# Optimization experiments

Hardware: AMD Instinct MI355X
Metric: run time of the kernel (lower is better)

The kernel has to match this reference:

```python
import jax, jax.numpy as jnp
import numpy as np

DIM = 192
HEADS = 8
EPS = 1e-12  # torch F.normalize eps


def setup_inputs() -> dict:
    key = jax.random.key(0)
    k1, k2, k3, k4 = jax.random.split(key, 4)
    b, c, h, w = 2, DIM, 256, 256
    x = jax.random.normal(k1, (b, c, h, w), dtype=jnp.float32)
    # 1x1 conv weights stored as (out, in)
    qkv_w = jax.random.normal(k2, (3 * c, c), dtype=jnp.float32) * (1.0 / np.sqrt(c))
    # depthwise 3x3, groups = 3c -> OIHW with I=1
    dw_w = jax.random.normal(k3, (3 * c, 1, 3, 3), dtype=jnp.float32) * (1.0 / 3.0)
    proj_w = jax.random.normal(k4, (c, c), dtype=jnp.float32) * (1.0 / np.sqrt(c))
    temperature = jnp.ones((HEADS, 1, 1), dtype=jnp.float32)
    return {"x": x, "qkv_w": qkv_w, "dw_w": dw_w, "proj_w": proj_w,
            "temperature": temperature}


def _l2norm(t):
    n = jnp.sqrt(jnp.sum(t * t, axis=-1, keepdims=True))
    return t / jnp.maximum(n, EPS)


def reference(x, qkv_w, dw_w, proj_w, temperature):
    b, c, h, w = x.shape
    # 1x1 conv (pointwise) -> depthwise 3x3 conv
    qkv = jnp.einsum('oc,bchw->bohw', qkv_w, x)  # (b, 3c, h, w)
    qkv = jax.lax.conv_general_dilated(
        qkv, dw_w, window_strides=(1, 1), padding='SAME',
        feature_group_count=3 * c,
        dimension_numbers=('NCHW', 'OIHW', 'NCHW'))
    q, k, v = jnp.split(qkv, 3, axis=1)
    # faithful reshape: full C channels per head, spatial dim split by heads
    q = q.reshape(b, HEADS, c, -1)
    k = k.reshape(b, HEADS, c, -1)
    v = v.reshape(b, HEADS, c, -1)
    q = _l2norm(q)
    k = _l2norm(k)
    attn = jnp.einsum('bhcn,bhdn->bhcd', q, k) * temperature  # (b,H,c,c)
    attn = jax.nn.softmax(attn, axis=-1)
    out = jnp.einsum('bhcd,bhdn->bhcn', attn, v)
    out = out.reshape(b, c, h, w)
    out = jnp.einsum('oc,bchw->bohw', proj_w, out)
    return out
```

## Files before the change

kernel.cpp:

```cpp
#include <hip/hip_runtime.h>
#include <math.h>

typedef unsigned short u16;
typedef unsigned int   u32;
typedef short bf16x8 __attribute__((ext_vector_type(8)));
typedef float f32x4  __attribute__((ext_vector_type(4)));

#define MFMA16(a,b,c) __builtin_amdgcn_mfma_f32_16x16x32_bf16((a),(b),(c),0,0,0)

__device__ __forceinline__ float bf2f(u16 h){ u32 u=((u32)h)<<16; return __uint_as_float(u); }
__device__ __forceinline__ u16 f2bf(float f){ u32 u=__float_as_uint(f); return (u16)((u+0x7fffu+((u>>16)&1u))>>16); }

__device__ __forceinline__ void gl2lds(const u16* g, u16* l){
  __builtin_amdgcn_global_load_lds((const __attribute__((address_space(1))) u32*)g,
                                   (__attribute__((address_space(3))) u32*)l, 16, 0, 0);
}
__device__ __forceinline__ void stc(u16* p, float v){ *p = f2bf(v); }
__device__ __forceinline__ void stc(float* p, float v){ *p = v; }
__device__ __forceinline__ void ld4(const float* p, float* v){ float4 x=*(const float4*)p; v[0]=x.x;v[1]=x.y;v[2]=x.z;v[3]=x.w; }
__device__ __forceinline__ void ld4(const u16* p, float* v){ ushort4 x=*(const ushort4*)p; v[0]=bf2f(x.x);v[1]=bf2f(x.y);v[2]=bf2f(x.z);v[3]=bf2f(x.w); }

__device__ __forceinline__ int xcd_remap(){
  int gx = gridDim.x, gy = gridDim.y;
  int lin = blockIdx.x + gx*(blockIdx.y + gy*blockIdx.z);
  int nwg = gx*gy*gridDim.z;
  if (nwg & 7) return lin;
  int q = nwg >> 3;
  return (lin & 7)*q + (lin >> 3);
}

__global__ void prep_kernel(const float* __restrict__ qkv_w, const float* __restrict__ proj_w,
                            u16* __restrict__ wq, u16* __restrict__ wp, float* __restrict__ norms){
  int i = blockIdx.x*256 + threadIdx.x;
  if (i < 110592) wq[i] = f2bf(qkv_w[i]);
  else if (i < 147456) wp[i-110592] = f2bf(proj_w[i-110592]);
  else if (i < 156672) norms[i-147456] = 0.f;
}

template<typename TIN>
__global__ __launch_bounds__(256) void transpose_kernel(
    const TIN* __restrict__ in, u16* __restrict__ out,
    long in_hi, long in_lo, long out_slab, int in_pitch)
{
  __shared__ float tile[64][65];
  const int t = threadIdx.x;
  const int z = blockIdx.z;
  const TIN* ip = in + (long)(z>>3)*in_hi + (long)(z&7)*in_lo;
  u16* op = out + (long)z*out_slab;
  const int s0 = blockIdx.x*64, c0 = blockIdx.y*64;
  const int rl = t>>4, cc = (t&15)*4;
#pragma unroll
  for (int rr=0; rr<4; rr++){
    int row = rr*16 + rl;
    float v[4];
    ld4(ip + (long)(c0+row)*in_pitch + s0 + cc, v);
    tile[row][cc+0]=v[0]; tile[row][cc+1]=v[1]; tile[row][cc+2]=v[2]; tile[row][cc+3]=v[3];
  }
  __syncthreads();
#pragma unroll
  for (int wr=0; wr<4; wr++){
    int sl = wr*16 + rl;
    ushort4 s;
    s.x = f2bf(tile[cc+0][sl]); s.y = f2bf(tile[cc+1][sl]);
    s.z = f2bf(tile[cc+2][sl]); s.w = f2bf(tile[cc+3][sl]);
    *(ushort4*)(op + (long)(s0+sl)*192 + c0 + cc) = s;
  }
}

template<typename TC>
__global__ __launch_bounds__(256) void gemm_nt_kernel(
    const u16* __restrict__ A, const u16* __restrict__ B, TC* __restrict__ C,
    int M, long sB, long sC)
{
  __shared__ __align__(16) u16 As[128*32];
  __shared__ __align__(16) u16 Bs[128*32];
  const int t = threadIdx.x, w = t>>6, l = t&63;
  const int wrk = xcd_remap();
  const int mt = wrk % gridDim.x;
  const int rest = wrk / gridDim.x;
  const int nt = rest % gridDim.y, bz = rest / gridDim.y;
  const int m0 = mt*128, n0 = nt*128;
  const u16* Bb = B + (long)bz*sB + (long)n0*192;
  const int rq = t>>2, qq = (t&3)*8;
  int ar0 = m0 + rq;      if (ar0 >= M) ar0 = M-1;
  int ar1 = m0 + 64 + rq; if (ar1 >= M) ar1 = M-1;
  f32x4 acc[4][4];
#pragma unroll
  for (int i=0;i<4;i++)
#pragma unroll
    for (int j=0;j<4;j++) acc[i][j] = f32x4{0.f,0.f,0.f,0.f};

  for (int k0=0; k0<192; k0+=32){
    __syncthreads();
    gl2lds(A + (long)ar0*192 + k0 + qq, As + t*8);
    gl2lds(A + (long)ar1*192 + k0 + qq, As + (256+t)*8);
    gl2lds(Bb + (long)rq*192 + k0 + qq, Bs + t*8);
    gl2lds(Bb + (long)(64+rq)*192 + k0 + qq, Bs + (256+t)*8);
    __syncthreads();
    const u16* ap = As + ((w>>1)*64 + (l&15))*32 + (l>>4)*8;
    const u16* bp = Bs + ((w&1)*64 + (l&15))*32 + (l>>4)*8;
    bf16x8 a[4], b[4];
#pragma unroll
    for (int i=0;i<4;i++){ a[i] = *(const bf16x8*)(ap + i*512); b[i] = *(const bf16x8*)(bp + i*512); }
#pragma unroll
    for (int i=0;i<4;i++)
#pragma unroll
      for (int j=0;j<4;j++) acc[i][j] = MFMA16(a[i], b[j], acc[i][j]);
  }
  const int mw = m0 + (w>>1)*64, nw = n0 + (w&1)*64;
  TC* Cb = C + (long)bz*sC;
#pragma unroll
  for (int i=0;i<4;i++){
#pragma unroll
    for (int r=0;r<4;r++){
      int row = mw + i*16 + (l>>4)*4 + r;
      if (row < M){
        TC* cp = Cb + (long)row*65536 + nw + (l&15);
#pragma unroll
        for (int j=0;j<4;j++) stc(cp + j*16, acc[i][j][r]);
      }
    }
  }
}

__global__ __launch_bounds__(256) void dwconv_kernel(
    const u16* __restrict__ in, const float* __restrict__ w9s,
    u16* __restrict__ out, float* __restrict__ norms)
{
  const int bo = blockIdx.x >> 2;
  const int rg = blockIdx.x & 3;
  const int o  = bo % 576;
  const int t = threadIdx.x, wv = t>>6, l = t&63;
  const u16* ip = in + (long)bo*65536L + l*4;
  u16* op = out + (long)bo*65536L + l*4;
  float w[9];
#pragma unroll
  for (int i=0;i<9;i++) w[i] = w9s[o*9+i];
  const int r0 = rg*64 + wv*16;
  float ap0=0.f,ap1=0.f,ap2=0.f,ap3=0.f;
  float ac0=0.f,ac1=0.f,ac2=0.f,ac3=0.f;
  float an0,an1,an2,an3;
  float ss = 0.f;
#pragma unroll
  for (int it=0; it<18; ++it){
    const int g = r0 - 1 + it;
    float v0,v1,v2,v3;
    if (g>=0 && g<256){
      ushort4 u = *(const ushort4*)(ip + g*256);
      v0=bf2f(u.x); v1=bf2f(u.y); v2=bf2f(u.z); v3=bf2f(u.w);
    } else { v0=0.f; v1=0.f; v2=0.f; v3=0.f; }
    float sl = __shfl(v3, (l+63)&63);
    float sr = __shfl(v0, (l+1)&63);
    const float lf  = (l==0)  ? 0.f : sl;
    const float rgt = (l==63) ? 0.f : sr;
    ap0 = fmaf(w[6],lf, fmaf(w[7],v0, fmaf(w[8],v1, ap0)));
    ap1 = fmaf(w[6],v0, fmaf(w[7],v1, fmaf(w[8],v2, ap1)));
    ap2 = fmaf(w[6],v1, fmaf(w[7],v2, fmaf(w[8],v3, ap2)));
    ap3 = fmaf(w[6],v2, fmaf(w[7],v3, fmaf(w[8],rgt, ap3)));
    if (it >= 2){
      ushort4 s;
      s.x = f2bf(ap0); s.y = f2bf(ap1); s.z = f2bf(ap2); s.w = f2bf(ap3);
      *(ushort4*)(op + (g-1)*256) = s;
      ss = fmaf(ap0,ap0, fmaf(ap1,ap1, fmaf(ap2,ap2, fmaf(ap3,ap3, ss))));
    }
    ac0 = fmaf(w[3],lf, fmaf(w[4],v0, fmaf(w[5],v1, ac0)));
    ac1 = fmaf(w[3],v0, fmaf(w[4],v1, fmaf(w[5],v2, ac1)));
    ac2 = fmaf(w[3],v1, fmaf(w[4],v2, fmaf(w[5],v3, ac2)));
    ac3 = fmaf(w[3],v2, fmaf(w[4],v3, fmaf(w[5],rgt, ac3)));
    an0 = fmaf(w[0],lf, fmaf(w[1],v0, w[2]*v1));
    an1 = fmaf(w[0],v0, fmaf(w[1],v1, w[2]*v2));
    an2 = fmaf(w[0],v1, fmaf(w[1],v2, w[2]*v3));
    an3 = fmaf(w[0],v2, fmaf(w[1],v3, w[2]*rgt));
    ap0=ac0; ap1=ac1; ap2=ac2; ap3=ac3;
    ac0=an0; ac1=an1; ac2=an2; ac3=an3;
  }
#pragma unroll
  for (int off=32; off>=1; off>>=1) ss += __shfl_xor(ss, off);
  if (o < 384 && l == 0){
    atomicAdd(&norms[bo*8 + (r0>>5)], ss);
  }
}

__global__ __launch_bounds__(256) void gemm_qk_kernel(
    const u16* __restrict__ conv, float* __restrict__ part)
{
  __shared__ __align__(16) u16 As[64*64];
  __shared__ __align__(16) u16 Bs[64*64];
  const int t = threadIdx.x, w = t>>6, l = t&63;
  const int wrk = xcd_remap();
  const int mt = wrk % 3;
  const int rest = wrk / 3;
  const int nt = rest % 3, z = rest / 3;
  const int bh = z>>3, sl = z&7;
  const int b = bh>>3, h = bh&7;
  const u16* Q  = conv + (long)b*37748736L + (long)h*1572864L;
  const u16* Kp = Q + 12582912L;
  const int m0 = mt*64, n0 = nt*64;
  const int rq = t>>3, qq = (t&7)*8;
  const long qo0 = (long)(m0+rq)*8192 + qq;
  const long qo1 = (long)(m0+32+rq)*8192 + qq;
  const long ko0 = (long)(n0+rq)*8192 + qq;
  const long ko1 = (long)(n0+32+rq)*8192 + qq;
  f32x4 acc[2][2];
#pragma unroll
  for (int i=0;i<2;i++)
#pragma unroll
    for (int j=0;j<2;j++) acc[i][j] = f32x4{0.f,0.f,0.f,0.f};
  const int kbeg = sl*1024;
  for (int k0=kbeg; k0<kbeg+1024; k0+=64){
    __syncthreads();
    gl2lds(Q  + qo0 + k0, As + t*8);
    gl2lds(Q  + qo1 + k0, As + (256+t)*8);
    gl2lds(Kp + ko0 + k0, Bs + t*8);
    gl2lds(Kp + ko1 + k0, Bs + (256+t)*8);
    __syncthreads();
    const u16* ap = As + ((w>>1)*32 + (l&15))*64 + (l>>4)*8;
    const u16* bp = Bs + ((w&1)*32 + (l&15))*64 + (l>>4)*8;
#pragma unroll
    for (int ks=0; ks<2; ks++){
      bf16x8 a0 = *(const bf16x8*)(ap + ks*32);
      bf16x8 a1 = *(const bf16x8*)(ap + 1024 + ks*32);
      bf16x8 b0 = *(const bf16x8*)(bp + ks*32);
      bf16x8 b1 = *(const bf16x8*)(bp + 1024 + ks*32);
      acc[0][0]=MFMA16(a0,b0,acc[0][0]); acc[0][1]=MFMA16(a0,b1,acc[0][1]);
      acc[1][0]=MFMA16(a1,b0,acc[1][0]); acc[1][1]=MFMA16(a1,b1,acc[1][1]);
    }
  }
  float* P = part + (long)z*36864L;
  const int mw = m0 + (w>>1)*32, nw = n0 + (w&1)*32;
#pragma unroll
  for (int i=0;i<2;i++)
#pragma unroll
    for (int j=0;j<2;j++)
#pragma unroll
      for (int r=0;r<4;r++)
        P[(long)(mw + i*16 + (l>>4)*4 + r)*192 + nw + j*16 + (l&15)] = acc[i][j][r];
}

__global__ __launch_bounds__(256) void softmax_kernel(
    const float* __restrict__ part, const float* __restrict__ temp,
    const float* __restrict__ norms, u16* __restrict__ attn)
{
  const int t = threadIdx.x, wv = t>>6, l = t&63;
  const int rg = blockIdx.x*4 + wv;
  const int bh = rg/192, r = rg - bh*192;
  const int b = bh>>3, h = bh&7;
  const float tp = temp[h];
  const float sq = norms[(b*576 + 24*h + (r>>3))*8 + (r&7)];
  const float invq = 1.f/fmaxf(sqrtf(sq), 1e-12f);
  const float* P = part + (long)bh*8L*36864L + (long)r*192;
  float lv[3];
#pragma unroll
  for (int j=0;j<3;j++){
    int col = l + j*64;
    float s = 0.f;
#pragma unroll
    for (int ks=0; ks<8; ks++) s += P[(long)ks*36864L + col];
    float sk = norms[(b*576 + 192 + 24*h + (col>>3))*8 + (col&7)];
    float invk = 1.f/fmaxf(sqrtf(sk), 1e-12f);
    lv[j] = s*invq*invk*tp;
  }
  float mx = fmaxf(lv[0], fmaxf(lv[1], lv[2]));
#pragma unroll
  for (int o=32;o>=1;o>>=1) mx = fmaxf(mx, __shfl_xor(mx, o));
  float e[3], sum = 0.f;
#pragma unroll
  for (int j=0;j<3;j++){ e[j] = expf(lv[j]-mx); sum += e[j]; }
#pragma unroll
  for (int o=32;o>=1;o>>=1) sum += __shfl_xor(sum, o);
  const float inv = 1.f/sum;
  u16* ap = attn + (long)bh*36864L + (long)r*192;
#pragma unroll
  for (int j=0;j<3;j++) ap[l + j*64] = f2bf(e[j]*inv);
}

__global__ __launch_bounds__(256) void gemm_av_kernel(
    const u16* __restrict__ VT, const u16* __restrict__ attn, u16* __restrict__ out_sc)
{
  __shared__ __align__(16) char smem[69632];
  u16* As = (u16*)smem;
  u16* Bs = (u16*)(smem + 8192);
  const int t = threadIdx.x, w = t>>6, l = t&63;
  const int wrk = xcd_remap();
  const int mt = wrk % 64;
  const int rest = wrk / 64;
  const int nt = rest % 2, bh = rest / 2;
  const int b = bh>>3, h = bh&7;
  const u16* Av = VT + (long)bh*1572864L;
  const u16* Bt = attn + (long)bh*36864L;
  const int m0 = mt*128, n0 = nt*128;
  const int rq = t>>2, qq = (t&3)*8;
  int br0 = n0 + rq;      if (br0 > 191) br0 = 191;
  int br1 = n0 + 64 + rq; if (br1 > 191) br1 = 191;
  f32x4 acc[4][4];
#pragma unroll
  for (int i=0;i<4;i++)
#pragma unroll
    for (int j=0;j<4;j++) acc[i][j] = f32x4{0.f,0.f,0.f,0.f};
  for (int k0=0; k0<192; k0+=32){
    __syncthreads();
    gl2lds(Av + (long)(m0+rq)*192 + k0 + qq, As + t*8);
    gl2lds(Av + (long)(m0+64+rq)*192 + k0 + qq, As + (256+t)*8);
    gl2lds(Bt + (long)br0*192 + k0 + qq, Bs + t*8);
    gl2lds(Bt + (long)br1*192 + k0 + qq, Bs + (256+t)*8);
    __syncthreads();
    const u16* ap = As + ((w>>1)*64 + (l&15))*32 + (l>>4)*8;
    const u16* bp = Bs + ((w&1)*64 + (l&15))*32 + (l>>4)*8;
    bf16x8 a[4], bb[4];
#pragma unroll
    for (int i=0;i<4;i++){ a[i] = *(const bf16x8*)(ap + i*512); bb[i] = *(const bf16x8*)(bp + i*512); }
#pragma unroll
    for (int i=0;i<4;i++)
#pragma unroll
      for (int j=0;j<4;j++) acc[i][j] = MFMA16(a[i], bb[j], acc[i][j]);
  }
  __syncthreads();
  float* wb = (float*)smem + w*4352;
#pragma unroll
  for (int i=0;i<4;i++)
#pragma unroll
    for (int j=0;j<4;j++)
#pragma unroll
      for (int r=0;r<4;r++)
        wb[(i*16 + (l>>4)*4 + r)*68 + j*16 + (l&15)] = acc[i][j][r];
  __syncthreads();
  const int c0w = nt*128 + (w&1)*64;
  if (c0w < 192){
    const int cb = 24*h + (c0w>>3);
    const int mw = m0 + (w>>1)*64;
    u16* ob = out_sc + (long)b*12582912L + cb;
    const int nl0 = l>>3, sb = l&7;
#pragma unroll
    for (int ri=0; ri<8; ri++){
      int nl = ri*8 + nl0;
      const float* src = wb + nl*68 + sb;
      u32 d0 = (u32)f2bf(src[0])  | ((u32)f2bf(src[8])  << 16);
      u32 d1 = (u32)f2bf(src[16]) | ((u32)f2bf(src[24]) << 16);
      u32 d2 = (u32)f2bf(src[32]) | ((u32)f2bf(src[40]) << 16);
      u32 d3 = (u32)f2bf(src[48]) | ((u32)f2bf(src[56]) << 16);
      *(uint4*)(ob + ((long)sb*8192 + mw + nl)*192) = make_uint4(d0,d1,d2,d3);
    }
  }
}

extern "C" void kernel_launch(void* const* d_in, const int* in_sizes, int n_in,
                              void* d_out, int out_size, void* d_ws, size_t ws_size,
                              hipStream_t stream)
{
  const float* x      = (const float*)d_in[0];
  const float* qkv_w  = (const float*)d_in[1];
  const float* dw_w   = (const float*)d_in[2];
  const float* proj_w = (const float*)d_in[3];
  const float* temp   = (const float*)d_in[4];
  float* out = (float*)d_out;

  char* ws = (char*)d_ws;
  u16*   xT      = (u16*)(ws + 0);
  u16*   conv    = (u16*)(ws + 0);
  u16*   qkv_raw = (u16*)(ws + 150994944);
  u16*   VT      = (u16*)(ws + 150994944);
  u16*   out_sc  = (u16*)(ws + 201326592);
  float* part    = (float*)(ws + 251658240);
  u16*   attn    = (u16*)(ws + 270532608);
  u16*   wq_bf   = (u16*)(ws + 301989888);
  u16*   wp_bf   = (u16*)(ws + 302211072);
  float* norms   = (float*)(ws + 302284800);

  prep_kernel<<<dim3(612), 256, 0, stream>>>(qkv_w, proj_w, wq_bf, wp_bf, norms);

  transpose_kernel<float><<<dim3(1024, 3, 2), 256, 0, stream>>>(
      x, xT, 0L, 12582912L, 12582912L, 65536);

  gemm_nt_kernel<u16><<<dim3(5, 512, 2), 256, 0, stream>>>(
      wq_bf, xT, qkv_raw, 576, 12582912L, 37748736L);

  dwconv_kernel<<<dim3(1152*4), 256, 0, stream>>>(qkv_raw, dw_w, conv, norms);

  transpose_kernel<u16><<<dim3(128, 3, 16), 256, 0, stream>>>(
      conv + 25165824L, VT, 37748736L, 1572864L, 1572864L, 8192);

  gemm_qk_kernel<<<dim3(3, 3, 128), 256, 0, stream>>>(conv, part);

  softmax_kernel<<<dim3(768), 256, 0, stream>>>(part, temp, norms, attn);

  gemm_av_kernel<<<dim3(64, 2, 16), 256, 0, stream>>>(VT, attn, out_sc);

  gemm_nt_kernel<float><<<dim3(2, 512, 2), 256, 0, stream>>>(
      wp_bf, out_sc, out, 192, 12582912L, 12582912L);
}
```

Baseline: 464.0 us.

## Fuse input transpose into QKV GEMM and widen depthwise conv per-thread work

Removes the separate fp32-to-bf16 transpose of x by having the QKV GEMM load fp32 x tiles directly into swizzled LDS and convert them to bf16 when building B fragments. This drops a full write and read of the transposed input. The depthwise conv now processes 8 columns per thread over 16 rows with half the blocks, and writes the norm partials directly instead of using atomics. The trade-off is twice the LDS traffic for the fp32 B tile plus per-element conversion inside the GEMM inner loop.

```diff
diff --git a/kernel.cpp b/kernel.cpp
--- a/kernel.cpp
+++ b/kernel.cpp
@@ -5,6 +5,7 @@
 typedef unsigned int   u32;
 typedef short bf16x8 __attribute__((ext_vector_type(8)));
 typedef float f32x4  __attribute__((ext_vector_type(4)));
+typedef u16 u16x8 __attribute__((ext_vector_type(8)));
 
 #define MFMA16(a,b,c) __builtin_amdgcn_mfma_f32_16x16x32_bf16((a),(b),(c),0,0,0)
 
@@ -37,15 +38,14 @@
   else if (i < 156672) norms[i-147456] = 0.f;
 }
 
-template<typename TIN>
 __global__ __launch_bounds__(256) void transpose_kernel(
-    const TIN* __restrict__ in, u16* __restrict__ out,
+    const u16* __restrict__ in, u16* __restrict__ out,
     long in_hi, long in_lo, long out_slab, int in_pitch)
 {
   __shared__ float tile[64][65];
   const int t = threadIdx.x;
   const int z = blockIdx.z;
-  const TIN* ip = in + (long)(z>>3)*in_hi + (long)(z&7)*in_lo;
+  const u16* ip = in + (long)(z>>3)*in_hi + (long)(z&7)*in_lo;
   u16* op = out + (long)z*out_slab;
   const int s0 = blockIdx.x*64, c0 = blockIdx.y*64;
   const int rl = t>>4, cc = (t&15)*4;
@@ -64,6 +64,77 @@
     s.x = f2bf(tile[cc+0][sl]); s.y = f2bf(tile[cc+1][sl]);
     s.z = f2bf(tile[cc+2][sl]); s.w = f2bf(tile[cc+3][sl]);
     *(ushort4*)(op + (long)(s0+sl)*192 + c0 + cc) = s;
+  }
+}
+
+__global__ __launch_bounds__(256) void gemm_qkv_kernel(
+    const u16* __restrict__ A, const float* __restrict__ X, u16* __restrict__ C)
+{
+  __shared__ __align__(16) u16 As[128*32];
+  __shared__ __align__(16) float Bs[32*128];
+  const int t = threadIdx.x, w = t>>6, l = t&63;
+  const int wrk = xcd_remap();
+  const int mt = wrk % 5;
+  const int rest = wrk / 5;
+  const int nt = rest % 512, bz = rest / 512;
+  const int m0 = mt*128, n0 = nt*128;
+  const float* Xb = X + (long)bz*12582912L + n0;
+  const int rq = t>>2, qq = (t&3)*8;
+  int ar0 = m0 + rq;      if (ar0 >= 576) ar0 = 575;
+  int ar1 = m0 + 64 + rq; if (ar1 >= 576) ar1 = 575;
+  const int brow = t>>5;
+  const int bcs0 = t&31;
+  f32x4 acc[4][4];
+#pragma unroll
+  for (int i=0;i<4;i++)
+#pragma unroll
+    for (int j=0;j<4;j++) acc[i][j] = f32x4{0.f,0.f,0.f,0.f};
+
+  for (int k0=0; k0<192; k0+=32){
+    __syncthreads();
+    gl2lds(A + (long)ar0*192 + k0 + qq, As + t*8);
+    gl2lds(A + (long)ar1*192 + k0 + qq, As + (256+t)*8);
+#pragma unroll
+    for (int i=0;i<4;i++){
+      const int r  = i*8 + brow;
+      const int cs = bcs0 ^ (i<<2);
+      gl2lds((const u16*)(Xb + (long)(k0+r)*65536 + cs*4),
+             (u16*)Bs + (i*256+t)*8);
+    }
+    __syncthreads();
+    const u16* ap = As + ((w>>1)*64 + (l&15))*32 + (l>>4)*8;
+    const int kg = l>>4;
+    const int colb = (w&1)*64 + (l&15);
+    bf16x8 a[4], b[4];
+#pragma unroll
+    for (int i=0;i<4;i++) a[i] = *(const bf16x8*)(ap + i*512);
+#pragma unroll
+    for (int j=0;j<4;j++){
+      const int col = colb + j*16;
+      const float* bp = Bs + kg*1024 + ((((col>>2) ^ (kg<<2))<<2) + (col&3));
+      bf16x8 bv;
+#pragma unroll
+      for (int jj=0;jj<8;jj++) bv[jj] = (short)f2bf(bp[jj*128]);
+      b[j] = bv;
+    }
+#pragma unroll
+    for (int i=0;i<4;i++)
+#pragma unroll
+      for (int j=0;j<4;j++) acc[i][j] = MFMA16(a[i], b[j], acc[i][j]);
+  }
+  const int mw = m0 + (w>>1)*64, nw = n0 + (w&1)*64;
+  u16* Cb = C + (long)bz*37748736L;
+#pragma unroll
+  for (int i=0;i<4;i++){
+#pragma unroll
+    for (int r=0;r<4;r++){
+      int row = mw + i*16 + (l>>4)*4 + r;
+      if (row < 576){
+        u16* cp = Cb + (long)row*65536 + nw + (l&15);
+#pragma unroll
+        for (int j=0;j<4;j++) stc(cp + j*16, acc[i][j][r]);
+      }
+    }
   }
 }
 
@@ -127,58 +198,59 @@
     const u16* __restrict__ in, const float* __restrict__ w9s,
     u16* __restrict__ out, float* __restrict__ norms)
 {
-  const int bo = blockIdx.x >> 2;
-  const int rg = blockIdx.x & 3;
+  const int bo = blockIdx.x >> 1;
+  const int half = blockIdx.x & 1;
   const int o  = bo % 576;
   const int t = threadIdx.x, wv = t>>6, l = t&63;
-  const u16* ip = in + (long)bo*65536L + l*4;
-  u16* op = out + (long)bo*65536L + l*4;
+  const int q = l&31;
+  const int r0 = half*128 + wv*32 + (l>>5)*16;
+  const u16* ip = in + (long)bo*65536L + q*8;
+  u16* op = out + (long)bo*65536L + q*8;
   float w[9];
 #pragma unroll
   for (int i=0;i<9;i++) w[i] = w9s[o*9+i];
-  const int r0 = rg*64 + wv*16;
-  float ap0=0.f,ap1=0.f,ap2=0.f,ap3=0.f;
-  float ac0=0.f,ac1=0.f,ac2=0.f,ac3=0.f;
-  float an0,an1,an2,an3;
+  float ap[8], ac[8], an[8];
+#pragma unroll
+  for (int c=0;c<8;c++){ ap[c]=0.f; ac[c]=0.f; }
   float ss = 0.f;
 #pragma unroll
   for (int it=0; it<18; ++it){
     const int g = r0 - 1 + it;
-    float v0,v1,v2,v3;
+    float v[8];
     if (g>=0 && g<256){
-      ushort4 u = *(const ushort4*)(ip + g*256);
-      v0=bf2f(u.x); v1=bf2f(u.y); v2=bf2f(u.z); v3=bf2f(u.w);
-    } else { v0=0.f; v1=0.f; v2=0.f; v3=0.f; }
-    float sl = __shfl(v3, (l+63)&63);
-    float sr = __shfl(v0, (l+1)&63);
-    const float lf  = (l==0)  ? 0.f : sl;
-    const float rgt = (l==63) ? 0.f : sr;
-    ap0 = fmaf(w[6],lf, fmaf(w[7],v0, fmaf(w[8],v1, ap0)));
-    ap1 = fmaf(w[6],v0, fmaf(w[7],v1, fmaf(w[8],v2, ap1)));
-    ap2 = fmaf(w[6],v1, fmaf(w[7],v2, fmaf(w[8],v3, ap2)));
-    ap3 = fmaf(w[6],v2, fmaf(w[7],v3, fmaf(w[8],rgt, ap3)));
+      u16x8 u = *(const u16x8*)(ip + g*256);
+#pragma unroll
+      for (int c=0;c<8;c++) v[c] = bf2f(u[c]);
+    } else {
+#pragma unroll
+      for (int c=0;c<8;c++) v[c]=0.f;
+    }
+    float slv = __shfl(v[7], (l+63)&63);
+    float srv = __shfl(v[0], (l+1)&63);
+    const float lf  = (q==0)  ? 0.f : slv;
+    const float rgt = (q==31) ? 0.f : srv;
+#pragma unroll
+    for (int c=0;c<8;c++){
+      const float le = (c==0) ? lf  : v[c-1];
+      const float mi = v[c];
+      const float ri = (c==7) ? rgt : v[c+1];
+      ap[c] = fmaf(w[6],le, fmaf(w[7],mi, fmaf(w[8],ri, ap[c])));
+      ac[c] = fmaf(w[3],le, fmaf(w[4],mi, fmaf(w[5],ri, ac[c])));
+      an[c] = fmaf(w[0],le, fmaf(w[1],mi, w[2]*ri));
+    }
     if (it >= 2){
-      ushort4 s;
-      s.x = f2bf(ap0); s.y = f2bf(ap1); s.z = f2bf(ap2); s.w = f2bf(ap3);
-      *(ushort4*)(op + (g-1)*256) = s;
-      ss = fmaf(ap0,ap0, fmaf(ap1,ap1, fmaf(ap2,ap2, fmaf(ap3,ap3, ss))));
-    }
-    ac0 = fmaf(w[3],lf, fmaf(w[4],v0, fmaf(w[5],v1, ac0)));
-    ac1 = fmaf(w[3],v0, fmaf(w[4],v1, fmaf(w[5],v2, ac1)));
-    ac2 = fmaf(w[3],v1, fmaf(w[4],v2, fmaf(w[5],v3, ac2)));
-    ac3 = fmaf(w[3],v2, fmaf(w[4],v3, fmaf(w[5],rgt, ac3)));
-    an0 = fmaf(w[0],lf, fmaf(w[1],v0, w[2]*v1));
-    an1 = fmaf(w[0],v0, fmaf(w[1],v1, w[2]*v2));
-    an2 = fmaf(w[0],v1, fmaf(w[1],v2, w[2]*v3));
-    an3 = fmaf(w[0],v2, fmaf(w[1],v3, w[2]*rgt));
-    ap0=ac0; ap1=ac1; ap2=ac2; ap3=ac3;
-    ac0=an0; ac1=an1; ac2=an2; ac3=an3;
+      u16x8 s;
+#pragma unroll
+      for (int c=0;c<8;c++){ s[c] = f2bf(ap[c]); ss = fmaf(ap[c],ap[c],ss); }
+      *(u16x8*)(op + (g-1)*256) = s;
+    }
+#pragma unroll
+    for (int c=0;c<8;c++){ ap[c]=ac[c]; ac[c]=an[c]; }
   }
 #pragma unroll
   for (int off=32; off>=1; off>>=1) ss += __shfl_xor(ss, off);
-  if (o < 384 && l == 0){
-    atomicAdd(&norms[bo*8 + (r0>>5)], ss);
-  }
+  if (o < 384 && l == 0)
+    norms[bo*8 + half*4 + wv] = ss;
 }
 
 __global__ __launch_bounds__(256) void gemm_qk_kernel(
@@ -355,7 +427,6 @@
   float* out = (float*)d_out;
 
   char* ws = (char*)d_ws;
-  u16*   xT      = (u16*)(ws + 0);
   u16*   conv    = (u16*)(ws + 0);
   u16*   qkv_raw = (u16*)(ws + 150994944);
   u16*   VT      = (u16*)(ws + 150994944);
@@ -368,15 +439,11 @@
 
   prep_kernel<<<dim3(612), 256, 0, stream>>>(qkv_w, proj_w, wq_bf, wp_bf, norms);
 
-  transpose_kernel<float><<<dim3(1024, 3, 2), 256, 0, stream>>>(
-      x, xT, 0L, 12582912L, 12582912L, 65536);
-
-  gemm_nt_kernel<u16><<<dim3(5, 512, 2), 256, 0, stream>>>(
-      wq_bf, xT, qkv_raw, 576, 12582912L, 37748736L);
-
-  dwconv_kernel<<<dim3(1152*4), 256, 0, stream>>>(qkv_raw, dw_w, conv, norms);
-
-  transpose_kernel<u16><<<dim3(128, 3, 16), 256, 0, stream>>>(
+  gemm_qkv_kernel<<<dim3(5, 512, 2), 256, 0, stream>>>(wq_bf, x, qkv_raw);
+
+  dwconv_kernel<<<dim3(1152*2), 256, 0, stream>>>(qkv_raw, dw_w, conv, norms);
+
+  transpose_kernel<<<dim3(128, 3, 16), 256, 0, stream>>>(
       conv + 25165824L, VT, 37748736L, 1572864L, 1572864L, 8192);
 
   gemm_qk_kernel<<<dim3(3, 3, 128), 256, 0, stream>>>(conv, part);
```

New measurement: 463.3 us. No clear change (-0.2%).
